# Kernel optimization log

Hardware: AMD Instinct MI355X
Metric: run time of the kernel (lower is better)

## Reference

```python
import jax, jax.numpy as jnp
import numpy as np

B, S, D = 4, 4096, 128

def setup_inputs() -> dict:
    key = jax.random.key(0)
    kq, kk, kv = jax.random.split(key, 3)
    q = jax.random.normal(kq, (B, S, D), dtype=jnp.float32)
    k = jax.random.normal(kk, (B, S, D), dtype=jnp.float32)
    v = jax.random.normal(kv, (B, S, D), dtype=jnp.float32)
    return {"q": q, "k": k, "v": v}

def reference(q, k, v):
    d_model = q.shape[-1]
    scale = 1.0 / jnp.sqrt(jnp.asarray(d_model, q.dtype))
    # [B, S, S] scores
    scores = jnp.einsum('bqd,bkd->bqk', q, k) * scale
    s = q.shape[1]
    causal = jnp.tril(jnp.ones((s, s), dtype=bool))
    neg_inf = jnp.asarray(-jnp.inf, scores.dtype)
    scores = jnp.where(causal[None, :, :], scores, neg_inf)
    attn = jax.nn.softmax(scores, axis=-1)
    return jnp.einsum('bqk,bkd->bqd', attn, v)
```

## Files before the change

### kernel.cpp

```cpp
#include <hip/hip_runtime.h>


#define B_   4
#define S_   4096
#define D_   128
#define BN   64
#define NT_  64
#define QT_  32
#define NCHB 119
#define BLOB_SHORTS 16384
#define MASKVAL (-1.0e30f)
#define DEFER_THR 8.0f

typedef __attribute__((ext_vector_type(8))) short bf16x8;
typedef __attribute__((ext_vector_type(4))) float f32x4;

__device__ __host__ __forceinline__ constexpr int chunks_of(int t) { return (2 * t + 11) / 10; }
constexpr int nchb_calc() { int s = 0; for (int t = 0; t < QT_; ++t) s += chunks_of(t); return s; }
static_assert(nchb_calc() == NCHB, "chunk count mismatch");

__device__ __forceinline__ short f2bf(float x) {
    unsigned u = __builtin_bit_cast(unsigned, x);
    unsigned r = (u + 0x7fffu + ((u >> 16) & 1u)) >> 16;
    return (short)r;
}
__device__ __forceinline__ float ex2(float x) { return __builtin_amdgcn_exp2f(x); }
__device__ __forceinline__ unsigned pkbf(float lo, float hi) {
    return (unsigned)(unsigned short)f2bf(lo) | ((unsigned)(unsigned short)f2bf(hi) << 16);
}
__device__ __forceinline__ void gl_lds16(const short* g, short* l) {
    __builtin_amdgcn_global_load_lds(
        (const __attribute__((address_space(1))) unsigned int*)g,
        (__attribute__((address_space(3))) unsigned int*)l, 16, 0, 0);
}

__global__ __launch_bounds__(256) void prep(const float* __restrict__ Qg,
                                            const float* __restrict__ Kg,
                                            const float* __restrict__ Vg,
                                            short* __restrict__ Qbf,
                                            short* __restrict__ KV)
{
    __shared__ short vt[64][40];
    const int id  = blockIdx.x;
    const int tid = threadIdx.x;
    const float SC = 0.12751740f;

    if (id < 1024) {
        const int b = id & 3, tile = (id >> 2) & 63, q4 = id >> 8;
        const int n = q4 * 16 + (tid >> 4);
        const int G = tid & 15;
        const size_t rowoff = ((size_t)b * S_ + (size_t)tile * 64 + n) * D_ + G * 8;
        short* blob = KV + (size_t)(b * NT_ + tile) * BLOB_SHORTS;
        {
            float4 a = *reinterpret_cast<const float4*>(Qg + rowoff);
            float4 c = *reinterpret_cast<const float4*>(Qg + rowoff + 4);
            bf16x8 v;
            v[0] = f2bf(a.x * SC); v[1] = f2bf(a.y * SC); v[2] = f2bf(a.z * SC); v[3] = f2bf(a.w * SC);
            v[4] = f2bf(c.x * SC); v[5] = f2bf(c.y * SC); v[6] = f2bf(c.z * SC); v[7] = f2bf(c.w * SC);
            *reinterpret_cast<bf16x8*>(Qbf + rowoff) = v;
        }
        {
            float4 a = *reinterpret_cast<const float4*>(Kg + rowoff);
            float4 c = *reinterpret_cast<const float4*>(Kg + rowoff + 4);
            bf16x8 v;
            v[0] = f2bf(a.x); v[1] = f2bf(a.y); v[2] = f2bf(a.z); v[3] = f2bf(a.w);
            v[4] = f2bf(c.x); v[5] = f2bf(c.y); v[6] = f2bf(c.z); v[7] = f2bf(c.w);
            const int p = (G & 8) | ((G & 7) ^ (n & 7));
            *reinterpret_cast<bf16x8*>(blob + n * 128 + p * 8) = v;
        }
    } else {
        const int u = id - 1024;
        const int b = u & 3, tile = (u >> 2) & 63, dq = u >> 8;
        short* blob = KV + (size_t)(b * NT_ + tile) * BLOB_SHORTS;
        {
            const int n = tid >> 2, c8 = tid & 3;
            const size_t off = ((size_t)b * S_ + (size_t)tile * 64 + n) * D_ + dq * 32 + c8 * 8;
            float4 a = *reinterpret_cast<const float4*>(Vg + off);
            float4 c = *reinterpret_cast<const float4*>(Vg + off + 4);
            bf16x8 v;
            v[0] = f2bf(a.x); v[1] = f2bf(a.y); v[2] = f2bf(a.z); v[3] = f2bf(a.w);
            v[4] = f2bf(c.x); v[5] = f2bf(c.y); v[6] = f2bf(c.z); v[7] = f2bf(c.w);
            *reinterpret_cast<bf16x8*>(&vt[n][c8 * 8]) = v;
        }
        __syncthreads();
        {
            const int dl = tid >> 3, G = tid & 7;
            const int d  = dq * 32 + dl;
            bf16x8 g;
#pragma unroll
            for (int i = 0; i < 8; ++i) g[i] = vt[G * 8 + i][dl];
            const int p = G ^ (d & 7);
            *reinterpret_cast<bf16x8*>(blob + 8192 + d * 64 + p * 8) = g;
        }
    }
}

template<bool SPLIT>
__global__ __launch_bounds__(512, 4) void fa_fwd(const short* __restrict__ Qbf,
                                                 const short* __restrict__ KV,
                                                 float* __restrict__ Og,
                                                 float* __restrict__ Op,
                                                 float* __restrict__ Ml)
{
    __shared__ short lkv[2][BLOB_SHORTS];

    const int tid  = threadIdx.x;
    const int wv   = tid >> 6;
    const int lane = tid & 63;
    const int m    = lane & 15;
    const int quad = lane >> 4;
    const int m7   = m & 7;

    int batch, t, lo, hi, chunk_id;
    {
        const int id = blockIdx.x;
        batch = id & 3;
        int u = id >> 2;
        if (SPLIT) {
            int tt = QT_ - 1, base = 0, rt;
            for (;;) { rt = chunks_of(tt); if (u < base + rt) break; base += rt; --tt; }
            t = tt;
            const int r  = u - base;
            const int nk = 2 * t + 2;
            lo = r * nk / rt;
            hi = (r + 1) * nk / rt;
            chunk_id = batch * NCHB + u;
        } else {
            t  = QT_ - 1 - u;
            lo = 0; hi = 2 * t + 2; chunk_id = 0;
        }
        if (lo >= hi) return;
    }

    bf16x8 qf[4];
    {
        const short* qp = Qbf + ((size_t)batch * S_ + (size_t)t * 128 + wv * 16 + m) * D_ + quad * 8;
#pragma unroll
        for (int c = 0; c < 4; ++c)
            qf[c] = *reinterpret_cast<const bf16x8*>(qp + c * 32);
    }

    f32x4 acc[8];
#pragma unroll
    for (int i = 0; i < 8; ++i) acc[i] = (f32x4){0.f, 0.f, 0.f, 0.f};
    float mrun = MASKVAL, lrun = 0.f;

    const size_t tilebase = (size_t)batch * NT_ * BLOB_SHORTS;
    const int qtop = t * 128 + wv * 16 + 15;
#define STAGE(KT, BUF) do {                                                   \
        const short* g_ = KV + tilebase + (size_t)(KT) * BLOB_SHORTS + tid * 8;\
        short* l_ = (BUF) + tid * 8;                                          \
        _Pragma("unroll")                                                     \
        for (int c_ = 0; c_ < 4; ++c_)                                        \
            gl_lds16(g_ + c_ * 4096, l_ + c_ * 4096);                         \
    } while (0)

    STAGE(lo, lkv[0]);

    for (int kt = lo; kt < hi; ++kt) {
        const short* cur = lkv[(kt - lo) & 1];
        short* nxt = lkv[(kt - lo + 1) & 1];
        __syncthreads();
        if (kt + 1 < hi) STAGE(kt + 1, nxt);

        if (kt * 64 > qtop) continue;

        const short* lk = cur;
        const short* lv = cur + 8192;

        f32x4 st[4];
#pragma unroll
        for (int nt = 0; nt < 4; ++nt) st[nt] = (f32x4){0.f, 0.f, 0.f, 0.f};
        __builtin_amdgcn_s_setprio(1);
#pragma unroll
        for (int c = 0; c < 4; ++c) {
            const int p = ((c >> 1) * 8) | ((((c & 1) * 4) | quad) ^ m7);
#pragma unroll
            for (int nt = 0; nt < 4; ++nt) {
                bf16x8 kf = *reinterpret_cast<const bf16x8*>(lk + nt * 2048 + m * 128 + p * 8);
                st[nt] = __builtin_amdgcn_mfma_f32_16x16x32_bf16(kf, qf[c], st[nt], 0, 0, 0);
            }
        }
        __builtin_amdgcn_s_setprio(0);

        if (kt >= 2 * t) {
            const int kbase = (kt - 2 * t) * 64;
            const int qloc  = wv * 16 + m;
#pragma unroll
            for (int nt = 0; nt < 4; ++nt)
#pragma unroll
                for (int r = 0; r < 4; ++r)
                    if (kbase + nt * 16 + quad * 4 + r > qloc) st[nt][r] = MASKVAL;
        }

        float mx = MASKVAL;
#pragma unroll
        for (int nt = 0; nt < 4; ++nt)
#pragma unroll
            for (int r = 0; r < 4; ++r) mx = fmaxf(mx, st[nt][r]);
        mx = fmaxf(mx, __shfl_xor(mx, 16));
        mx = fmaxf(mx, __shfl_xor(mx, 32));
        if (__any(mx - mrun > DEFER_THR)) {
            const float mnew = fmaxf(mrun, mx);
            const float al   = ex2(mrun - mnew);
            mrun = mnew;
            lrun *= al;
#pragma unroll
            for (int r = 0; r < 4; ++r) {
                float alq = __shfl(al, quad * 4 + r);
#pragma unroll
                for (int ct = 0; ct < 8; ++ct) acc[ct][r] *= alq;
            }
        }
        float sum = 0.f;
#pragma unroll
        for (int nt = 0; nt < 4; ++nt)
#pragma unroll
            for (int r = 0; r < 4; ++r) {
                float pv = ex2(st[nt][r] - mrun);
                st[nt][r] = pv;
                sum += pv;
            }
        lrun += sum;

        const int srcA = ((quad & 1) << 5) + m;
        const int srcB = srcA + 16;
        const bool loq = quad < 2;
#pragma unroll
        for (int ks = 0; ks < 2; ++ks) {
            unsigned pk0 = pkbf(st[2 * ks][0],     st[2 * ks][1]);
            unsigned pk1 = pkbf(st[2 * ks][2],     st[2 * ks][3]);
            unsigned pk2 = pkbf(st[2 * ks + 1][0], st[2 * ks + 1][1]);
            unsigned pk3 = pkbf(st[2 * ks + 1][2], st[2 * ks + 1][3]);
            unsigned w0a = __shfl((int)pk0, srcA);
            unsigned w0b = __shfl((int)pk2, srcA);
            unsigned w1a = __shfl((int)pk1, srcA);
            unsigned w1b = __shfl((int)pk3, srcA);
            unsigned w2a = __shfl((int)pk0, srcB);
            unsigned w2b = __shfl((int)pk2, srcB);
            unsigned w3a = __shfl((int)pk1, srcB);
            unsigned w3b = __shfl((int)pk3, srcB);
            int4 wi;
            wi.x = (int)(loq ? w0a : w0b);
            wi.y = (int)(loq ? w1a : w1b);
            wi.z = (int)(loq ? w2a : w2b);
            wi.w = (int)(loq ? w3a : w3b);
            bf16x8 pf = __builtin_bit_cast(bf16x8, wi);
            const int p = (ks * 4 + quad) ^ m7;
            __builtin_amdgcn_s_setprio(1);
#pragma unroll
            for (int ct = 0; ct < 8; ++ct) {
                bf16x8 vf = *reinterpret_cast<const bf16x8*>(lv + ct * 1024 + m * 64 + p * 8);
                acc[ct] = __builtin_amdgcn_mfma_f32_16x16x32_bf16(pf, vf, acc[ct], 0, 0, 0);
            }
            __builtin_amdgcn_s_setprio(0);
        }
    }
#undef STAGE

    lrun += __shfl_xor(lrun, 16);
    lrun += __shfl_xor(lrun, 32);

    const int row0 = wv * 16 + quad * 4;
    if (SPLIT) {
        float* ob = Op + (size_t)chunk_id * (128 * D_);
#pragma unroll
        for (int r = 0; r < 4; ++r)
#pragma unroll
            for (int ct = 0; ct < 8; ++ct)
                ob[(row0 + r) * D_ + ct * 16 + m] = acc[ct][r];
        if (lane < 16) {
            float* mlb = Ml + (size_t)chunk_id * (128 * 2) + (wv * 16 + lane) * 2;
            mlb[0] = mrun;
            mlb[1] = lrun;
        }
    } else {
        const float inv = 1.0f / lrun;
        const size_t obase = ((size_t)batch * S_ + (size_t)t * 128 + row0) * D_;
#pragma unroll
        for (int r = 0; r < 4; ++r) {
            float invq = __shfl(inv, quad * 4 + r);
#pragma unroll
            for (int ct = 0; ct < 8; ++ct)
                Og[obase + (size_t)r * D_ + ct * 16 + m] = acc[ct][r] * invq;
        }
    }
}

__global__ __launch_bounds__(256) void fa_merge(const float* __restrict__ Op,
                                                const float* __restrict__ Ml,
                                                float* __restrict__ Og)
{
    const int x   = blockIdx.x;
    const int btq = x >> 4;
    const int oct = x & 15;
    const int t   = btq & (QT_ - 1);
    const int b   = btq >> 5;
    const int rt  = chunks_of(t);
    int base = 0;
    for (int tt = QT_ - 1; tt > t; --tt) base += chunks_of(tt);
    const int cbase = b * NCHB + base;
    const int row = oct * 8 + (threadIdx.x >> 5);
    const int cg  = threadIdx.x & 31;

    float mr_[7], lr_[7];
    float mg = MASKVAL;
#pragma unroll
    for (int r = 0; r < 7; ++r)
        if (r < rt) {
            float2 ml2 = *reinterpret_cast<const float2*>(
                Ml + (size_t)(cbase + r) * (128 * 2) + row * 2);
            mr_[r] = ml2.x;
            lr_[r] = ml2.y;
            mg = fmaxf(mg, mr_[r]);
        }
    float l = 0.f;
    f32x4 a = (f32x4){0.f, 0.f, 0.f, 0.f};
#pragma unroll
    for (int r = 0; r < 7; ++r)
        if (r < rt) {
            float w = ex2(mr_[r] - mg);
            l += lr_[r] * w;
            a += w * *reinterpret_cast<const f32x4*>(
                Op + (size_t)(cbase + r) * (128 * D_) + row * D_ + cg * 4);
        }
    *reinterpret_cast<f32x4*>(Og + (size_t)btq * (128 * D_) + row * D_ + cg * 4) = a * (1.0f / l);
}

extern "C" void kernel_launch(void* const* d_in, const int* in_sizes, int n_in,
                              void* d_out, int out_size, void* d_ws, size_t ws_size,
                              hipStream_t stream) {
    const float* q = (const float*)d_in[0];
    const float* k = (const float*)d_in[1];
    const float* v = (const float*)d_in[2];
    float* o = (float*)d_out;

    const size_t QBF_BYTES = (size_t)B_ * S_ * D_ * 2;
    const size_t KV_BYTES  = (size_t)B_ * NT_ * BLOB_SHORTS * 2;
    const size_t PREFIX    = QBF_BYTES + KV_BYTES;
    const int    NCH       = B_ * NCHB;
    const size_t O_FLOATS  = (size_t)NCH * 128 * D_;
    const size_t ML_FLOATS = (size_t)NCH * 128 * 2;
    const size_t NEEDED    = PREFIX + (O_FLOATS + ML_FLOATS) * sizeof(float);

    char* ws = (char*)d_ws;
    short* Qbf = (short*)ws;
    short* KV  = (short*)(ws + QBF_BYTES);

    prep<<<dim3(2048), 256, 0, stream>>>(q, k, v, Qbf, KV);

    if (ws_size >= NEEDED) {
        float* Op = (float*)(ws + PREFIX);
        float* Ml = Op + O_FLOATS;
        fa_fwd<true><<<dim3(NCH), 512, 0, stream>>>(Qbf, KV, nullptr, Op, Ml);
        fa_merge<<<dim3(B_ * QT_ * 16), 256, 0, stream>>>(Op, Ml, o);
    } else {
        fa_fwd<false><<<dim3(B_ * QT_), 512, 0, stream>>>(Qbf, KV, o, nullptr, nullptr);
    }
}
```

Baseline: 117.4 us.

## Store split partials as packed bf16, use hardware bf16 pack, defer row-max shuffles

Split-KV partial outputs are now written as packed bf16 pairs with vectorized 16-byte stores, and the merge kernel reads and unpacks them. This halves the partial-output traffic between the forward and merge kernels. The bf16 packing of P now uses the v_cvt_pk_bf16_f32 instruction instead of manual integer rounding. The cross-lane row-max shuffles move inside the rescale branch. Partial accumulators lose precision by being stored in bf16, and the merge writes become scattered scalar stores.

New measurement: 113.5 us (median of 2 runs). -3.3%, faster.

```diff
diff --git a/kernel.cpp b/kernel.cpp
--- a/kernel.cpp
+++ b/kernel.cpp
@@ -25,8 +25,10 @@
     return (short)r;
 }
 __device__ __forceinline__ float ex2(float x) { return __builtin_amdgcn_exp2f(x); }
-__device__ __forceinline__ unsigned pkbf(float lo, float hi) {
-    return (unsigned)(unsigned short)f2bf(lo) | ((unsigned)(unsigned short)f2bf(hi) << 16);
+__device__ __forceinline__ unsigned cvtpk(float lo, float hi) {
+    unsigned r;
+    asm("v_cvt_pk_bf16_f32 %0, %1, %2" : "=v"(r) : "v"(lo), "v"(hi));
+    return r;
 }
 __device__ __forceinline__ void gl_lds16(const short* g, short* l) {
     __builtin_amdgcn_global_load_lds(
@@ -99,7 +101,7 @@
 __global__ __launch_bounds__(512, 4) void fa_fwd(const short* __restrict__ Qbf,
                                                  const short* __restrict__ KV,
                                                  float* __restrict__ Og,
-                                                 float* __restrict__ Op,
+                                                 unsigned* __restrict__ Op,
                                                  float* __restrict__ Ml)
 {
     __shared__ short lkv[2][BLOB_SHORTS];
@@ -193,15 +195,15 @@
                     if (kbase + nt * 16 + quad * 4 + r > qloc) st[nt][r] = MASKVAL;
         }
 
-        float mx = MASKVAL;
-#pragma unroll
-        for (int nt = 0; nt < 4; ++nt)
-#pragma unroll
-            for (int r = 0; r < 4; ++r) mx = fmaxf(mx, st[nt][r]);
-        mx = fmaxf(mx, __shfl_xor(mx, 16));
-        mx = fmaxf(mx, __shfl_xor(mx, 32));
+        float t0 = fmaxf(fmaxf(st[0][0], st[0][1]), fmaxf(st[0][2], st[0][3]));
+        float t1 = fmaxf(fmaxf(st[1][0], st[1][1]), fmaxf(st[1][2], st[1][3]));
+        float t2 = fmaxf(fmaxf(st[2][0], st[2][1]), fmaxf(st[2][2], st[2][3]));
+        float t3 = fmaxf(fmaxf(st[3][0], st[3][1]), fmaxf(st[3][2], st[3][3]));
+        float mx = fmaxf(fmaxf(t0, t1), fmaxf(t2, t3));
         if (__any(mx - mrun > DEFER_THR)) {
-            const float mnew = fmaxf(mrun, mx);
+            float mw = fmaxf(mx, __shfl_xor(mx, 16));
+            mw = fmaxf(mw, __shfl_xor(mw, 32));
+            const float mnew = fmaxf(mrun, mw);
             const float al   = ex2(mrun - mnew);
             mrun = mnew;
             lrun *= al;
@@ -228,10 +230,10 @@
         const bool loq = quad < 2;
 #pragma unroll
         for (int ks = 0; ks < 2; ++ks) {
-            unsigned pk0 = pkbf(st[2 * ks][0],     st[2 * ks][1]);
-            unsigned pk1 = pkbf(st[2 * ks][2],     st[2 * ks][3]);
-            unsigned pk2 = pkbf(st[2 * ks + 1][0], st[2 * ks + 1][1]);
-            unsigned pk3 = pkbf(st[2 * ks + 1][2], st[2 * ks + 1][3]);
+            unsigned pk0 = cvtpk(st[2 * ks][0],     st[2 * ks][1]);
+            unsigned pk1 = cvtpk(st[2 * ks][2],     st[2 * ks][3]);
+            unsigned pk2 = cvtpk(st[2 * ks + 1][0], st[2 * ks + 1][1]);
+            unsigned pk3 = cvtpk(st[2 * ks + 1][2], st[2 * ks + 1][3]);
             unsigned w0a = __shfl((int)pk0, srcA);
             unsigned w0b = __shfl((int)pk2, srcA);
             unsigned w1a = __shfl((int)pk1, srcA);
@@ -263,12 +265,16 @@
 
     const int row0 = wv * 16 + quad * 4;
     if (SPLIT) {
-        float* ob = Op + (size_t)chunk_id * (128 * D_);
-#pragma unroll
-        for (int r = 0; r < 4; ++r)
-#pragma unroll
-            for (int ct = 0; ct < 8; ++ct)
-                ob[(row0 + r) * D_ + ct * 16 + m] = acc[ct][r];
+        unsigned* ob = Op + (size_t)chunk_id * (128 * 64);
+#pragma unroll
+        for (int r = 0; r < 4; ++r) {
+            uint4 w;
+            w.x = cvtpk(acc[0][r], acc[1][r]);
+            w.y = cvtpk(acc[2][r], acc[3][r]);
+            w.z = cvtpk(acc[4][r], acc[5][r]);
+            w.w = cvtpk(acc[6][r], acc[7][r]);
+            *reinterpret_cast<uint4*>(ob + (row0 + r) * 64 + m * 4) = w;
+        }
         if (lane < 16) {
             float* mlb = Ml + (size_t)chunk_id * (128 * 2) + (wv * 16 + lane) * 2;
             mlb[0] = mrun;
@@ -287,7 +293,7 @@
     }
 }
 
-__global__ __launch_bounds__(256) void fa_merge(const float* __restrict__ Op,
+__global__ __launch_bounds__(256) void fa_merge(const unsigned* __restrict__ Op,
                                                 const float* __restrict__ Ml,
                                                 float* __restrict__ Og)
 {
@@ -301,7 +307,7 @@
     for (int tt = QT_ - 1; tt > t; --tt) base += chunks_of(tt);
     const int cbase = b * NCHB + base;
     const int row = oct * 8 + (threadIdx.x >> 5);
-    const int cg  = threadIdx.x & 31;
+    const int g   = threadIdx.x & 31;
 
     float mr_[7], lr_[7];
     float mg = MASKVAL;
@@ -315,16 +321,26 @@
             mg = fmaxf(mg, mr_[r]);
         }
     float l = 0.f;
-    f32x4 a = (f32x4){0.f, 0.f, 0.f, 0.f};
+    float a0 = 0.f, a1 = 0.f, a2 = 0.f, a3 = 0.f;
 #pragma unroll
     for (int r = 0; r < 7; ++r)
         if (r < rt) {
             float w = ex2(mr_[r] - mg);
             l += lr_[r] * w;
-            a += w * *reinterpret_cast<const f32x4*>(
-                Op + (size_t)(cbase + r) * (128 * D_) + row * D_ + cg * 4);
-        }
-    *reinterpret_cast<f32x4*>(Og + (size_t)btq * (128 * D_) + row * D_ + cg * 4) = a * (1.0f / l);
+            uint2 pk = *reinterpret_cast<const uint2*>(
+                Op + (size_t)(cbase + r) * (128 * 64) + row * 64 + g * 2);
+            a0 += w * __builtin_bit_cast(float, pk.x << 16);
+            a1 += w * __builtin_bit_cast(float, pk.x & 0xffff0000u);
+            a2 += w * __builtin_bit_cast(float, pk.y << 16);
+            a3 += w * __builtin_bit_cast(float, pk.y & 0xffff0000u);
+        }
+    const float inv = 1.0f / l;
+    float* og = Og + (size_t)btq * (128 * D_) + row * D_;
+    const int d0 = 64 * (g & 1) + (g >> 1);
+    og[d0]      = a0 * inv;
+    og[d0 + 16] = a1 * inv;
+    og[d0 + 32] = a2 * inv;
+    og[d0 + 48] = a3 * inv;
 }
 
 extern "C" void kernel_launch(void* const* d_in, const int* in_sizes, int n_in,
@@ -339,9 +355,9 @@
     const size_t KV_BYTES  = (size_t)B_ * NT_ * BLOB_SHORTS * 2;
     const size_t PREFIX    = QBF_BYTES + KV_BYTES;
     const int    NCH       = B_ * NCHB;
-    const size_t O_FLOATS  = (size_t)NCH * 128 * D_;
-    const size_t ML_FLOATS = (size_t)NCH * 128 * 2;
-    const size_t NEEDED    = PREFIX + (O_FLOATS + ML_FLOATS) * sizeof(float);
+    const size_t O_BYTES   = (size_t)NCH * 128 * 64 * 4;
+    const size_t ML_BYTES  = (size_t)NCH * 128 * 2 * 4;
+    const size_t NEEDED    = PREFIX + O_BYTES + ML_BYTES;
 
     char* ws = (char*)d_ws;
     short* Qbf = (short*)ws;
@@ -350,8 +366,8 @@
     prep<<<dim3(2048), 256, 0, stream>>>(q, k, v, Qbf, KV);
 
     if (ws_size >= NEEDED) {
-        float* Op = (float*)(ws + PREFIX);
-        float* Ml = Op + O_FLOATS;
+        unsigned* Op = (unsigned*)(ws + PREFIX);
+        float* Ml = (float*)(ws + PREFIX + O_BYTES);
         fa_fwd<true><<<dim3(NCH), 512, 0, stream>>>(Qbf, KV, nullptr, Op, Ml);
         fa_merge<<<dim3(B_ * QT_ * 16), 256, 0, stream>>>(Op, Ml, o);
     } else {
```
